# Kernel tuning notes

Measured on AMD Instinct MI355X. Metric: run time of the kernel, lower is better.

Reference implementation:

```python
import jax, jax.numpy as jnp
import numpy as np

D = 256; NH = 8; NL = 4; NP = 4; NLAYERS = 6; DFF = 1024; DH = D // NH
B = 2
SHAPES = [(128, 128), (64, 64), (32, 32), (16, 16)]
S_TOTAL = sum(h * w for h, w in SHAPES)  # 21760


def setup_inputs() -> dict:
    key = jax.random.key(0)
    ks = iter(jax.random.split(key, 64))
    inp = {}
    for l, (h, w) in enumerate(SHAPES):
        inp[f"src{l}"] = jax.random.normal(next(ks), (B, D, h, w), jnp.float32)
        inp[f"pos{l}"] = jax.random.normal(next(ks), (B, D, h, w), jnp.float32)
    def p(shape):
        return jax.random.normal(next(ks), shape, jnp.float32) * 0.02
    inp["level_embed"] = p((NL, D))
    inp["Woff"] = p((NLAYERS, D, NH * NL * NP * 2)); inp["boff"] = p((NLAYERS, NH * NL * NP * 2))
    inp["Wattn"] = p((NLAYERS, D, NH * NL * NP)); inp["battn"] = p((NLAYERS, NH * NL * NP))
    inp["Wval"] = p((NLAYERS, D, D)); inp["bval"] = p((NLAYERS, D))
    inp["Wout"] = p((NLAYERS, D, D)); inp["bout"] = p((NLAYERS, D))
    inp["ln1_s"] = jnp.ones((NLAYERS, D)); inp["ln1_b"] = jnp.zeros((NLAYERS, D))
    inp["W1"] = p((NLAYERS, D, DFF)); inp["b1"] = p((NLAYERS, DFF))
    inp["W2"] = p((NLAYERS, DFF, D)); inp["b2"] = p((NLAYERS, D))
    inp["ln2_s"] = jnp.ones((NLAYERS, D)); inp["ln2_b"] = jnp.zeros((NLAYERS, D))
    return inp


def _layer_norm(x, s, b, eps=1e-5):
    m = jnp.mean(x, -1, keepdims=True)
    v = jnp.mean((x - m) ** 2, -1, keepdims=True)
    return (x - m) * jax.lax.rsqrt(v + eps) * s + b


def _ref_points(batch):
    # masks are all-False -> valid_ratios == 1, so reference points are just
    # normalized pixel centers, identical across the level axis.
    refs = []
    for h, w in SHAPES:
        yy, xx = jnp.meshgrid((jnp.arange(h) + 0.5) / h, (jnp.arange(w) + 0.5) / w, indexing="ij")
        refs.append(jnp.stack([xx.ravel(), yy.ravel()], -1))
    ref = jnp.concatenate(refs, 0)  # [S, 2] (x, y)
    return jnp.broadcast_to(ref[None, :, None, :], (batch, S_TOTAL, NL, 2))


def _ms_deform_attn(query, ref, src, Woff, boff, Wattn, battn, Wval, bval, Wout, bout):
    Bq, S, _ = query.shape
    value = (src @ Wval + bval).reshape(Bq, S, NH, DH)
    off = (query @ Woff + boff).reshape(Bq, S, NH, NL, NP, 2)
    aw = jax.nn.softmax((query @ Wattn + battn).reshape(Bq, S, NH, NL * NP), -1)
    aw = aw.reshape(Bq, S, NH, NL, NP)
    norm = jnp.array([[w, h] for h, w in SHAPES], dtype=query.dtype)  # [NL,2] = (W,H)
    loc = ref[:, :, None, :, None, :] + off / norm[None, None, None, :, None, :]  # [B,S,NH,NL,NP,2]
    out = jnp.zeros((Bq, NH, S, DH), query.dtype)
    start = 0
    for l, (h, w) in enumerate(SHAPES):
        v = value[:, start:start + h * w].transpose(0, 2, 1, 3)  # [B,NH,h*w,DH]
        start += h * w
        # grid_sample align_corners=False convention
        x = loc[:, :, :, l, :, 0] * w - 0.5  # [B,S,NH,NP]
        y = loc[:, :, :, l, :, 1] * h - 0.5
        x0 = jnp.floor(x); y0 = jnp.floor(y)
        lx = x - x0; ly = y - y0
        x0i = x0.astype(jnp.int32); y0i = y0.astype(jnp.int32)
        def tr(a):  # [B,S,NH,NP] -> [B,NH,S*NP,1]
            return a.transpose(0, 2, 1, 3).reshape(Bq, NH, S * NP, 1)
        def gather(xi, yi):
            ok = (xi >= 0) & (xi < w) & (yi >= 0) & (yi < h)
            idx = jnp.clip(yi, 0, h - 1) * w + jnp.clip(xi, 0, w - 1)
            idx = idx.transpose(0, 2, 1, 3).reshape(Bq, NH, S * NP)
            g = jnp.take_along_axis(v, idx[..., None], axis=2)  # [B,NH,S*NP,DH]
            return g * tr(ok).astype(v.dtype)  # zero padding outside
        samp = (tr((1 - lx) * (1 - ly)) * gather(x0i, y0i)
                + tr(lx * (1 - ly)) * gather(x0i + 1, y0i)
                + tr((1 - lx) * ly) * gather(x0i, y0i + 1)
                + tr(lx * ly) * gather(x0i + 1, y0i + 1))
        samp = (samp * tr(aw[:, :, :, l])).reshape(Bq, NH, S, NP, DH).sum(3)
        out = out + samp
    out = out.transpose(0, 2, 1, 3).reshape(Bq, S, D)
    return out @ Wout + bout


def _forward(srcs, poss, level_embed, Woff, boff, Wattn, battn, Wval, bval, Wout, bout,
             ln1_s, ln1_b, W1, b1, W2, b2, ln2_s, ln2_b):
    bsz = srcs[0].shape[0]
    src_flat = jnp.concatenate([s.reshape(bsz, D, -1).transpose(0, 2, 1) for s in srcs], 1)
    pos_flat = jnp.concatenate(
        [p.reshape(bsz, D, -1).transpose(0, 2, 1) + level_embed[l] for l, p in enumerate(poss)], 1)
    ref = _ref_points(bsz)
    out = src_flat
    for i in range(NLAYERS):
        q = out + pos_flat
        attn = _ms_deform_attn(q, ref, out, Woff[i], boff[i], Wattn[i], battn[i],
                               Wval[i], bval[i], Wout[i], bout[i])
        out = _layer_norm(out + attn, ln1_s[i], ln1_b[i])
        ff = jax.nn.relu(out @ W1[i] + b1[i]) @ W2[i] + b2[i]
        out = _layer_norm(out + ff, ln2_s[i], ln2_b[i])
    return out  # memory: [B, S_TOTAL, D]


def reference(src0, src1, src2, src3, pos0, pos1, pos2, pos3, level_embed,
              Woff, boff, Wattn, battn, Wval, bval, Wout, bout,
              ln1_s, ln1_b, W1, b1, W2, b2, ln2_s, ln2_b):
    return _forward([src0, src1, src2, src3], [pos0, pos1, pos2, pos3], level_embed,
                    Woff, boff, Wattn, battn, Wval, bval, Wout, bout,
                    ln1_s, ln1_b, W1, b1, W2, b2, ln2_s, ln2_b)
```

## Files before the change

### kernel.cpp

```cpp
#include <hip/hip_runtime.h>
#include <math.h>

#define DMODEL 256
#define NHEADS 8
#define NLAY 6
#define DFF 1024
#define DHEAD 32
#define NB 2
#define STOT 21760
#define MTOT (NB * STOT)

typedef unsigned short u16;
typedef __attribute__((ext_vector_type(8))) short short8;
typedef __attribute__((ext_vector_type(4))) float floatx4;
typedef __attribute__((ext_vector_type(2))) float float2v;

__device__ __forceinline__ float bf2f(u16 h) {
    unsigned int u = ((unsigned int)h) << 16;
    return __uint_as_float(u);
}
__device__ __forceinline__ u16 f2bf(float f) {
    unsigned int u = __float_as_uint(f);
    u = u + 0x7fffu + ((u >> 16) & 1u);
    return (u16)(u >> 16);
}

__device__ __forceinline__ void pkfma(float2v& acc, float2v a, float2v b) {
    asm("v_pk_fma_f32 %0, %1, %2, %0" : "+v"(acc) : "v"(a), "v"(b));
}
__device__ __forceinline__ float2v unpk(unsigned int u) {
    float2v r;
    r.x = __uint_as_float(u << 16);
    r.y = __uint_as_float(u & 0xffff0000u);
    return r;
}

__device__ __forceinline__ void gload16(const u16* g, u16* l) {
    __builtin_amdgcn_global_load_lds(
        (const __attribute__((address_space(1))) unsigned int*)(g),
        (__attribute__((address_space(3))) unsigned int*)(l),
        16, 0, 0);
}

__global__ __launch_bounds__(256)
void biascat_kernel(const float* __restrict__ boff, const float* __restrict__ battn,
                    float* __restrict__ bias384)
{
    const int t = blockIdx.x * 256 + threadIdx.x;
    if (t >= NLAY * 384) return;
    const int i = t / 384, c = t - i * 384;
    bias384[t] = (c < 256) ? boff[i * 256 + c] : battn[i * 128 + (c - 256)];
}

__global__ __launch_bounds__(256)
void wtrans_kernel(const float* __restrict__ W, u16* __restrict__ Wt,
                   const int K, const int N, const long wstride, const long ostride)
{
    __shared__ float ts[32][33];
    W  += blockIdx.z * wstride;
    Wt += blockIdx.z * ostride;
    const int n0 = blockIdx.x * 32;
    const int k0 = blockIdx.y * 32;
    const int t = threadIdx.x;
    const int nl = t & 31, kl = t >> 5;
#pragma unroll
    for (int p = 0; p < 4; ++p) {
        const int k = kl + p * 8;
        ts[k][nl] = W[(long)(k0 + k) * N + n0 + nl];
    }
    __syncthreads();
    const int c = t & 31, r0 = t >> 5;
#pragma unroll
    for (int p = 0; p < 4; ++p) {
        const int r = r0 + p * 8;
        Wt[(long)(n0 + r) * K + k0 + c] = f2bf(ts[c][r]);
    }
}

__global__ __launch_bounds__(256)
void flatten_kernel(const float* __restrict__ src, const float* __restrict__ pos,
                    const float* __restrict__ le_row,
                    float* __restrict__ out, u16* __restrict__ outb,
                    u16* __restrict__ posb, u16* __restrict__ qb,
                    int HW, int start)
{
    __shared__ float ts[32][33];
    __shared__ float tp[32][33];
    const int b   = blockIdx.z;
    const int d0  = blockIdx.y * 32;
    const int hw0 = blockIdx.x * 32;
    const int t   = threadIdx.x;
    const int hwl = t & 31;
    const int dl  = t >> 5;
#pragma unroll
    for (int p = 0; p < 4; ++p) {
        const int dd = dl + p * 8;
        const int d  = d0 + dd;
        const long idx = ((long)(b * DMODEL + d)) * HW + hw0 + hwl;
        ts[dd][hwl] = src[idx];
        tp[dd][hwl] = pos[idx] + le_row[d];
    }
    __syncthreads();
    const int dl2  = t & 31;
    const int hwl2 = t >> 5;
#pragma unroll
    for (int p = 0; p < 4; ++p) {
        const int hh  = hwl2 + p * 8;
        const int tok = start + hw0 + hh;
        const long o  = ((long)(b * STOT + tok)) * DMODEL + d0 + dl2;
        const float v = ts[dl2][hh];
        const float pp = tp[dl2][hh];
        out[o]  = v;
        outb[o] = f2bf(v);
        posb[o] = f2bf(pp);
        qb[o]   = f2bf(v + pp);
    }
}

__global__ __launch_bounds__(256)
void mfma_gemm(const u16* __restrict__ A, const u16* __restrict__ Bt,
               const int ldb, const float* __restrict__ bias,
               u16* __restrict__ Cb, const int ldc, u16* __restrict__ Cb2,
               const int K, const int relu)
{
    __shared__ u16 As[128 * 32];
    __shared__ u16 Bs[128 * 32];
    const int tid  = threadIdx.x;
    const int wv   = tid >> 6;
    const int lane = tid & 63;
    const int m0 = blockIdx.y * 128;
    const int n0 = blockIdx.x * 128;
    const int wm = (wv & 1) * 64;
    const int wn = (wv >> 1) * 64;
    const int q   = lane >> 4;
    const int c16 = lane & 15;

    const int lrow = lane >> 2;
    const int lcol = (lane & 3) * 8;

    const u16* ag[2];
    const u16* bg[2];
#pragma unroll
    for (int it = 0; it < 2; ++it) {
        const int chunk = it * 4 + wv;
        const int row = chunk * 16 + lrow;
        ag[it] = A  + (long)(m0 + row) * K   + lcol;
        bg[it] = Bt + (long)(n0 + row) * ldb + lcol;
    }

    floatx4 acc[4][4];
#pragma unroll
    for (int i = 0; i < 4; ++i)
#pragma unroll
        for (int j = 0; j < 4; ++j)
            acc[i][j] = (floatx4){0.f, 0.f, 0.f, 0.f};

    for (int k0 = 0; k0 < K; k0 += 32) {
#pragma unroll
        for (int it = 0; it < 2; ++it) {
            const int chunk = it * 4 + wv;
            gload16(ag[it] + k0, &As[chunk * 512]);
            gload16(bg[it] + k0, &Bs[chunk * 512]);
        }
        __syncthreads();

        short8 af[4], bf[4];
#pragma unroll
        for (int i = 0; i < 4; ++i) {
            af[i] = *(const short8*)&As[(wm + i * 16 + c16) * 32 + q * 8];
            bf[i] = *(const short8*)&Bs[(wn + i * 16 + c16) * 32 + q * 8];
        }
#pragma unroll
        for (int i = 0; i < 4; ++i)
#pragma unroll
            for (int j = 0; j < 4; ++j)
                acc[i][j] = __builtin_amdgcn_mfma_f32_16x16x32_bf16(
                    af[i], bf[j], acc[i][j], 0, 0, 0);
        __syncthreads();
    }

    u16* cb  = Cb;
    int ldcb = ldc, csub = 0;
    if (Cb2 && n0 >= 256) { cb = Cb2; ldcb = 128; csub = 256; }

#pragma unroll
    for (int i = 0; i < 4; ++i) {
#pragma unroll
        for (int j = 0; j < 4; ++j) {
            const int col = n0 + wn + j * 16 + c16;
            const float bv = bias ? bias[col] : 0.f;
#pragma unroll
            for (int r = 0; r < 4; ++r) {
                const int row = m0 + wm + i * 16 + q * 4 + r;
                float v = acc[i][j][r] + bv;
                if (relu) v = fmaxf(v, 0.f);
                cb[(long)row * ldcb + col - csub] = f2bf(v);
            }
        }
    }
}

__device__ __forceinline__ void point_corners(
    float refx, float refy, unsigned int o2, float aP,
    int k, unsigned int base, float* w, unsigned int* o)
{
    const int lw = 128 >> k;
    const float flw = (float)lw;
    const float x = refx * flw - 0.5f + bf2f((u16)(o2 & 0xffffu));
    const float y = refy * flw - 0.5f + bf2f((u16)(o2 >> 16));
    const float x0f = floorf(x), y0f = floorf(y);
    const float lx = x - x0f, ly = y - y0f;
    const int x0 = (int)x0f, y0 = (int)y0f;
    const float wx0 = ((unsigned int)x0 < (unsigned int)lw) ? (1.f - lx) : 0.f;
    const float wx1 = ((unsigned int)(x0 + 1) < (unsigned int)lw) ? lx : 0.f;
    const float wy0 = ((unsigned int)y0 < (unsigned int)lw) ? (aP * (1.f - ly)) : 0.f;
    const float wy1 = ((unsigned int)(y0 + 1) < (unsigned int)lw) ? (aP * ly) : 0.f;
    const unsigned int xc0 = (unsigned int)(x0 & (lw - 1)) << 9;
    const unsigned int xc1 = (unsigned int)((x0 + 1) & (lw - 1)) << 9;
    const unsigned int r0 = (unsigned int)(y0 & (lw - 1)) << (16 - k);
    const unsigned int r1 = (unsigned int)((y0 + 1) & (lw - 1)) << (16 - k);
    w[0] = wy0 * wx0; o[0] = base + r0 + xc0;
    w[1] = wy0 * wx1; o[1] = base + r0 + xc1;
    w[2] = wy1 * wx0; o[2] = base + r1 + xc0;
    w[3] = wy1 * wx1; o[3] = base + r1 + xc1;
}

__global__ __launch_bounds__(256, 4)
void sample_kernel(const u16* __restrict__ value, const u16* __restrict__ offb,
                   const u16* __restrict__ logit, u16* __restrict__ sb)
{
    const int t  = threadIdx.x;
    const int wv = t >> 6;
    const int l  = t & 63;
    const int h  = l >> 3;
    const int u  = l & 7;
    const int blk = blockIdx.x * 4 + wv;
    const int b = blk / STOT;
    const int s = blk - b * STOT;

    float refx, refy;
    if (s < 16384) {
        const int yy = s >> 7, xx = s & 127;
        refx = (xx + 0.5f) * (1.f / 128.f); refy = (yy + 0.5f) * (1.f / 128.f);
    } else if (s < 20480) {
        const int sl = s - 16384; const int yy = sl >> 6, xx = sl & 63;
        refx = (xx + 0.5f) * (1.f / 64.f);  refy = (yy + 0.5f) * (1.f / 64.f);
    } else if (s < 21504) {
        const int sl = s - 20480; const int yy = sl >> 5, xx = sl & 31;
        refx = (xx + 0.5f) * (1.f / 32.f);  refy = (yy + 0.5f) * (1.f / 32.f);
    } else {
        const int sl = s - 21504; const int yy = sl >> 4, xx = sl & 15;
        refx = (xx + 0.5f) * (1.f / 16.f);  refy = (yy + 0.5f) * (1.f / 16.f);
    }

    const unsigned int* offp = (const unsigned int*)(offb + (long)blk * 256 + h * 32);
    const unsigned int o2_0 = offp[u];
    const unsigned int o2_1 = offp[u + 8];
    const u16* lp = logit + (long)blk * 128 + h * 16;
    const float l0 = bf2f(lp[u]);
    const float l1 = bf2f(lp[u + 8]);

    float m = fmaxf(l0, l1);
    m = fmaxf(m, __shfl_xor(m, 1));
    m = fmaxf(m, __shfl_xor(m, 2));
    m = fmaxf(m, __shfl_xor(m, 4));
    const float e0 = __expf(l0 - m);
    const float e1 = __expf(l1 - m);
    float se = e0 + e1;
    se += __shfl_xor(se, 1);
    se += __shfl_xor(se, 2);
    se += __shfl_xor(se, 4);
    const float inv = 1.f / se;
    const float aP0 = e0 * inv;
    const float aP1 = e1 * inv;

    const int k0 = u >> 2;
    const unsigned int LS0 = k0 ? 16384u : 0u;
    const unsigned int LS1 = k0 ? 21504u : 20480u;
    const unsigned int tb = (unsigned int)(b * STOT);
    const unsigned int hb64 = (unsigned int)(h * 64);
    const unsigned int base0 = (tb + LS0) * 512u + hb64;
    const unsigned int base1 = (tb + LS1) * 512u + hb64;

    float ww[8];
    unsigned int oo[8];
    point_corners(refx, refy, o2_0, aP0, k0,     base0, ww,     oo);
    point_corners(refx, refy, o2_1, aP1, k0 + 2, base1, ww + 4, oo + 4);

    const int sbase = l & 56;
    const unsigned int chb = (unsigned int)(u * 8);
    const char* vp = (const char*)value;
    float2v acc0; acc0.x = 0.f; acc0.y = 0.f;
    float2v acc1; acc1.x = 0.f; acc1.y = 0.f;

#pragma unroll
    for (int g = 0; g < 4; ++g) {
        float wB[16];
        unsigned int oB[16];
        uint2 dB[16];
#pragma unroll
        for (int pp = 0; pp < 4; ++pp) {
            const int p = g * 4 + pp;
            const int src = sbase + (p & 7);
            const int slotbase = (p >> 3) * 4;
#pragma unroll
            for (int c = 0; c < 4; ++c) {
                oB[pp * 4 + c] = (unsigned int)__shfl((int)oo[slotbase + c], src);
                wB[pp * 4 + c] = __shfl(ww[slotbase + c], src);
            }
        }
#pragma unroll
        for (int i = 0; i < 16; ++i)
            dB[i] = *(const uint2*)(vp + (oB[i] + chb));
#pragma unroll
        for (int i = 0; i < 16; ++i) {
            float2v w2; w2.x = wB[i]; w2.y = wB[i];
            pkfma(acc0, w2, unpk(dB[i].x));
            pkfma(acc1, w2, unpk(dB[i].y));
        }
    }

    ushort4 r;
    r.x = f2bf(acc0.x); r.y = f2bf(acc0.y);
    r.z = f2bf(acc1.x); r.w = f2bf(acc1.y);
    *(ushort4*)(sb + (long)blk * DMODEL + h * 32 + u * 4) = r;
}

__global__ __launch_bounds__(256)
void ln_kernel(float* __restrict__ out, u16* __restrict__ outb,
               u16* __restrict__ qb, const u16* __restrict__ posb,
               const u16* __restrict__ db,
               const float* __restrict__ gamma, const float* __restrict__ beta)
{
    const int wave = threadIdx.x >> 6;
    const int lane = threadIdx.x & 63;
    const long tok = (long)blockIdx.x * 4 + wave;
    float* op = out + tok * DMODEL + lane * 4;
    const float4 xo = *(const float4*)op;
    const ushort4 d4 = *(const ushort4*)(db + tok * DMODEL + lane * 4);
    float x[4] = {xo.x + bf2f(d4.x), xo.y + bf2f(d4.y),
                  xo.z + bf2f(d4.z), xo.w + bf2f(d4.w)};

    float sum = x[0] + x[1] + x[2] + x[3];
#pragma unroll
    for (int o = 32; o >= 1; o >>= 1) sum += __shfl_xor(sum, o);
    const float mean = sum * (1.f / 256.f);

    float vs = 0.f;
#pragma unroll
    for (int i = 0; i < 4; ++i) { const float d2 = x[i] - mean; vs += d2 * d2; }
#pragma unroll
    for (int o = 32; o >= 1; o >>= 1) vs += __shfl_xor(vs, o);
    const float rstd = rsqrtf(vs * (1.f / 256.f) + 1e-5f);

    const float4 g  = *(const float4*)(gamma + lane * 4);
    const float4 be = *(const float4*)(beta + lane * 4);
    float r[4];
    r[0] = (x[0] - mean) * rstd * g.x + be.x;
    r[1] = (x[1] - mean) * rstd * g.y + be.y;
    r[2] = (x[2] - mean) * rstd * g.z + be.z;
    r[3] = (x[3] - mean) * rstd * g.w + be.w;
    float4 rf; rf.x = r[0]; rf.y = r[1]; rf.z = r[2]; rf.w = r[3];
    *(float4*)op = rf;
    ushort4 rb;
    rb.x = f2bf(r[0]); rb.y = f2bf(r[1]); rb.z = f2bf(r[2]); rb.w = f2bf(r[3]);
    *(ushort4*)(outb + tok * DMODEL + lane * 4) = rb;
    if (qb) {
        const ushort4 p4 = *(const ushort4*)(posb + tok * DMODEL + lane * 4);
        ushort4 qv;
        qv.x = f2bf(r[0] + bf2f(p4.x));
        qv.y = f2bf(r[1] + bf2f(p4.y));
        qv.z = f2bf(r[2] + bf2f(p4.z));
        qv.w = f2bf(r[3] + bf2f(p4.w));
        *(ushort4*)(qb + tok * DMODEL + lane * 4) = qv;
    }
}

extern "C" void kernel_launch(void* const* d_in, const int* in_sizes, int n_in,
                              void* d_out, int out_size, void* d_ws, size_t ws_size,
                              hipStream_t stream)
{
    const float* src[4] = {(const float*)d_in[0], (const float*)d_in[2],
                           (const float*)d_in[4], (const float*)d_in[6]};
    const float* pos[4] = {(const float*)d_in[1], (const float*)d_in[3],
                           (const float*)d_in[5], (const float*)d_in[7]};
    const float* level_embed = (const float*)d_in[8];
    const float* Woff  = (const float*)d_in[9];
    const float* boff  = (const float*)d_in[10];
    const float* Wattn = (const float*)d_in[11];
    const float* battn = (const float*)d_in[12];
    const float* Wval  = (const float*)d_in[13];
    const float* bval  = (const float*)d_in[14];
    const float* Wout  = (const float*)d_in[15];
    const float* bout  = (const float*)d_in[16];
    const float* ln1s  = (const float*)d_in[17];
    const float* ln1b  = (const float*)d_in[18];
    const float* W1    = (const float*)d_in[19];
    const float* b1    = (const float*)d_in[20];
    const float* W2    = (const float*)d_in[21];
    const float* b2    = (const float*)d_in[22];
    const float* ln2s  = (const float*)d_in[23];
    const float* ln2b  = (const float*)d_in[24];

    float* out = (float*)d_out;
    const long MD = (long)MTOT * DMODEL;

    u16* outb = (u16*)d_ws;
    u16* posb = outb + MD;
    u16* qb   = posb + MD;
    u16* db   = qb + MD;
    u16* vb   = db + MD;
    u16* offb = vb + MD;
    u16* awb  = offb + MD;
    u16* sb   = awb + MD / 2;
    u16* hb   = vb;
    u16* wts  = vb + 4 * MD;
    u16* Wvalt = wts;
    u16* Wofat = Wvalt + 6L * 256 * 256;
    u16* Woutt = Wofat + 6L * 384 * 256;
    u16* W1t   = Woutt + 6L * 256 * 256;
    u16* W2t   = W1t   + 6L * 1024 * 256;
    float* bias384 = (float*)(W2t + 6L * 1024 * 256);

    biascat_kernel<<<9, 256, 0, stream>>>(boff, battn, bias384);
    wtrans_kernel<<<dim3(8, 8, 6),  256, 0, stream>>>(Wval,  Wvalt, 256, 256,
                                                      65536, 65536);
    wtrans_kernel<<<dim3(8, 8, 6),  256, 0, stream>>>(Woff,  Wofat, 256, 256,
                                                      65536, 98304);
    wtrans_kernel<<<dim3(4, 8, 6),  256, 0, stream>>>(Wattn, Wofat + 256 * 256,
                                                      256, 128, 32768, 98304);
    wtrans_kernel<<<dim3(8, 8, 6),  256, 0, stream>>>(Wout,  Woutt, 256, 256,
                                                      65536, 65536);
    wtrans_kernel<<<dim3(32, 8, 6), 256, 0, stream>>>(W1,    W1t, 256, 1024,
                                                      262144, 262144);
    wtrans_kernel<<<dim3(8, 32, 6), 256, 0, stream>>>(W2,    W2t, 1024, 256,
                                                      262144, 262144);

    {
        const int HW[4] = {16384, 4096, 1024, 256};
        const int ST[4] = {0, 16384, 20480, 21504};
        for (int l = 0; l < 4; ++l) {
            dim3 g(HW[l] / 32, DMODEL / 32, NB);
            flatten_kernel<<<g, 256, 0, stream>>>(src[l], pos[l],
                                                  level_embed + l * DMODEL,
                                                  out, outb, posb, qb, HW[l], ST[l]);
        }
    }

    const dim3 g2(2, MTOT / 128);
    const dim3 g3(3, MTOT / 128);
    const dim3 g8(8, MTOT / 128);

    for (int i = 0; i < NLAY; ++i) {
        const u16* Wv  = Wvalt + (long)i * 256 * 256;
        const u16* Wqa = Wofat + (long)i * 384 * 256;
        const u16* Wou = Woutt + (long)i * 256 * 256;
        const u16* W1i = W1t   + (long)i * 1024 * 256;
        const u16* W2i = W2t   + (long)i * 256 * 1024;
        const float* bv  = bval + (long)i * 256;
        const float* bqa = bias384 + (long)i * 384;
        const float* bou = bout + (long)i * 256;
        const float* b1i = b1   + (long)i * DFF;
        const float* b2i = b2   + (long)i * 256;

        mfma_gemm<<<g2, 256, 0, stream>>>(outb, Wv, 256, bv,
                                          vb, 256, nullptr, 256, 0);
        mfma_gemm<<<g3, 256, 0, stream>>>(qb, Wqa, 256, bqa,
                                          offb, 256, awb, 256, 0);
        sample_kernel<<<MTOT / 4, 256, 0, stream>>>(vb, offb, awb, sb);
        mfma_gemm<<<g2, 256, 0, stream>>>(sb, Wou, 256, bou,
                                          db, 256, nullptr, 256, 0);
        ln_kernel<<<MTOT / 4, 256, 0, stream>>>(out, outb, nullptr, nullptr, db,
                                                ln1s + (long)i * 256,
                                                ln1b + (long)i * 256);
        mfma_gemm<<<g8, 256, 0, stream>>>(outb, W1i, 256, b1i,
                                          hb, 1024, nullptr, 256, 1);
        mfma_gemm<<<g2, 256, 0, stream>>>(hb, W2i, 1024, b2i,
                                          db, 256, nullptr, 1024, 0);
        ln_kernel<<<MTOT / 4, 256, 0, stream>>>(out, outb, qb, posb, db,
                                                ln2s + (long)i * 256,
                                                ln2b + (long)i * 256);
    }
}
```

Measured before the change: 1.997 ms.

## Double-buffer GEMM LDS tiles and stage sampling weights in shared memory

The bf16 MFMA GEMM now keeps two LDS buffers, so the next K-slice loads while the current one is multiplied, and each iteration has one barrier instead of two. Separately, the deformable sampling kernel writes each head's corner weights and offsets to a shared-memory table and reads them back as uint4 vectors. This replaces many cross-lane shuffles per group. The cost is double the GEMM LDS footprint, about 17KB of extra LDS in the sampler, and a wave barrier, all of which may lower occupancy.

```diff
diff --git a/kernel.cpp b/kernel.cpp
--- a/kernel.cpp
+++ b/kernel.cpp
@@ -123,8 +123,8 @@
                u16* __restrict__ Cb, const int ldc, u16* __restrict__ Cb2,
                const int K, const int relu)
 {
-    __shared__ u16 As[128 * 32];
-    __shared__ u16 Bs[128 * 32];
+    __shared__ u16 As[2][128 * 32];
+    __shared__ u16 Bs[2][128 * 32];
     const int tid  = threadIdx.x;
     const int wv   = tid >> 6;
     const int lane = tid & 63;
@@ -148,6 +148,16 @@
         bg[it] = Bt + (long)(n0 + row) * ldb + lcol;
     }
 
+#define STAGE(buf, kk)                                          \
+    {                                                           \
+        _Pragma("unroll")                                       \
+        for (int it = 0; it < 2; ++it) {                        \
+            const int chunk = it * 4 + wv;                      \
+            gload16(ag[it] + (kk), &As[buf][chunk * 512]);      \
+            gload16(bg[it] + (kk), &Bs[buf][chunk * 512]);      \
+        }                                                       \
+    }
+
     floatx4 acc[4][4];
 #pragma unroll
     for (int i = 0; i < 4; ++i)
@@ -155,20 +165,23 @@
         for (int j = 0; j < 4; ++j)
             acc[i][j] = (floatx4){0.f, 0.f, 0.f, 0.f};
 
+    STAGE(0, 0);
+    __syncthreads();
+
+    int cur = 0;
     for (int k0 = 0; k0 < K; k0 += 32) {
-#pragma unroll
-        for (int it = 0; it < 2; ++it) {
-            const int chunk = it * 4 + wv;
-            gload16(ag[it] + k0, &As[chunk * 512]);
-            gload16(bg[it] + k0, &Bs[chunk * 512]);
+        const int nxt = k0 + 32;
+        if (nxt < K) {
+            if (cur) { STAGE(0, nxt); } else { STAGE(1, nxt); }
         }
-        __syncthreads();
-
+
+        const u16* Ab = &As[cur][0];
+        const u16* Bb = &Bs[cur][0];
         short8 af[4], bf[4];
 #pragma unroll
         for (int i = 0; i < 4; ++i) {
-            af[i] = *(const short8*)&As[(wm + i * 16 + c16) * 32 + q * 8];
-            bf[i] = *(const short8*)&Bs[(wn + i * 16 + c16) * 32 + q * 8];
+            af[i] = *(const short8*)&Ab[(wm + i * 16 + c16) * 32 + q * 8];
+            bf[i] = *(const short8*)&Bb[(wn + i * 16 + c16) * 32 + q * 8];
         }
 #pragma unroll
         for (int i = 0; i < 4; ++i)
@@ -177,7 +190,9 @@
                 acc[i][j] = __builtin_amdgcn_mfma_f32_16x16x32_bf16(
                     af[i], bf[j], acc[i][j], 0, 0, 0);
         __syncthreads();
-    }
+        cur ^= 1;
+    }
+#undef STAGE
 
     u16* cb  = Cb;
     int ldcb = ldc, csub = 0;
@@ -229,6 +244,8 @@
 void sample_kernel(const u16* __restrict__ value, const u16* __restrict__ offb,
                    const u16* __restrict__ logit, u16* __restrict__ sb)
 {
+    __shared__ unsigned int pwtab[4 * 8 * 132];
+
     const int t  = threadIdx.x;
     const int wv = t >> 6;
     const int l  = t & 63;
@@ -287,7 +304,24 @@
     point_corners(refx, refy, o2_0, aP0, k0,     base0, ww,     oo);
     point_corners(refx, refy, o2_1, aP1, k0 + 2, base1, ww + 4, oo + 4);
 
-    const int sbase = l & 56;
+    unsigned int* wbase = pwtab + (wv * 8 + h) * 132;
+    {
+        uint4 p0, p1, p2, p3;
+        p0.x = __float_as_uint(ww[0]); p0.y = oo[0];
+        p0.z = __float_as_uint(ww[1]); p0.w = oo[1];
+        p1.x = __float_as_uint(ww[2]); p1.y = oo[2];
+        p1.z = __float_as_uint(ww[3]); p1.w = oo[3];
+        p2.x = __float_as_uint(ww[4]); p2.y = oo[4];
+        p2.z = __float_as_uint(ww[5]); p2.w = oo[5];
+        p3.x = __float_as_uint(ww[6]); p3.y = oo[6];
+        p3.z = __float_as_uint(ww[7]); p3.w = oo[7];
+        *(uint4*)(wbase + u * 8)           = p0;
+        *(uint4*)(wbase + u * 8 + 4)       = p1;
+        *(uint4*)(wbase + (u + 8) * 8)     = p2;
+        *(uint4*)(wbase + (u + 8) * 8 + 4) = p3;
+    }
+    __builtin_amdgcn_wave_barrier();
+
     const unsigned int chb = (unsigned int)(u * 8);
     const char* vp = (const char*)value;
     float2v acc0; acc0.x = 0.f; acc0.y = 0.f;
@@ -295,28 +329,24 @@
 
 #pragma unroll
     for (int g = 0; g < 4; ++g) {
-        float wB[16];
-        unsigned int oB[16];
+        const uint4* gp = (const uint4*)(wbase + g * 32);
+        uint4 qq[8];
+#pragma unroll
+        for (int i = 0; i < 8; ++i) qq[i] = gp[i];
         uint2 dB[16];
 #pragma unroll
-        for (int pp = 0; pp < 4; ++pp) {
-            const int p = g * 4 + pp;
-            const int src = sbase + (p & 7);
-            const int slotbase = (p >> 3) * 4;
-#pragma unroll
-            for (int c = 0; c < 4; ++c) {
-                oB[pp * 4 + c] = (unsigned int)__shfl((int)oo[slotbase + c], src);
-                wB[pp * 4 + c] = __shfl(ww[slotbase + c], src);
-            }
+        for (int i = 0; i < 8; ++i) {
+            dB[2 * i]     = *(const uint2*)(vp + (qq[i].y + chb));
+            dB[2 * i + 1] = *(const uint2*)(vp + (qq[i].w + chb));
         }
 #pragma unroll
-        for (int i = 0; i < 16; ++i)
-            dB[i] = *(const uint2*)(vp + (oB[i] + chb));
-#pragma unroll
-        for (int i = 0; i < 16; ++i) {
-            float2v w2; w2.x = wB[i]; w2.y = wB[i];
-            pkfma(acc0, w2, unpk(dB[i].x));
-            pkfma(acc1, w2, unpk(dB[i].y));
+        for (int i = 0; i < 8; ++i) {
+            float2v wa; wa.x = __uint_as_float(qq[i].x); wa.y = wa.x;
+            pkfma(acc0, wa, unpk(dB[2 * i].x));
+            pkfma(acc1, wa, unpk(dB[2 * i].y));
+            float2v wb; wb.x = __uint_as_float(qq[i].z); wb.y = wb.x;
+            pkfma(acc0, wb, unpk(dB[2 * i + 1].x));
+            pkfma(acc1, wb, unpk(dB[2 * i + 1].y));
         }
     }
 
```

Measured after the change: 1.900 ms. -4.8%, faster.
